# Optimization experiments

Measured on AMD Instinct MI355X. Metric: run time of the kernel, lower is better.

The kernel has to match this reference:

```python
import jax, jax.numpy as jnp
import numpy as np

B, S, D = 2, 2048, 2048
NH, NKV, HD = 16, 4, 128
ROPE_BASE = 10000.0
NEG = -1e9


def _rope_tables(seq_len, dim):
    inv_freq = 1.0 / ROPE_BASE ** (jnp.arange(0, dim, 2, dtype=jnp.float32) / dim)
    t = jnp.arange(seq_len, dtype=jnp.float32)
    freqs = jnp.outer(t, inv_freq)                      # [S, dim/2]
    return jnp.cos(freqs), jnp.sin(freqs)


def _apply_rope(x, cos, sin):
    # x: [B, S, H, HD]; interleaved-pair rotation matching the original module
    x1 = x[..., ::2]
    x2 = x[..., 1::2]
    c = cos[None, :, None, :]
    s = sin[None, :, None, :]
    out1 = x1 * c - x2 * s
    out2 = x1 * s + x2 * c
    return jnp.stack([out1, out2], axis=-1).reshape(x.shape)


def setup_inputs() -> dict:
    key = jax.random.key(0)
    ks = jax.random.split(key, 5)
    x = jax.random.normal(ks[0], (B, S, D), dtype=jnp.float32)
    # causal additive mask [1, 1, S, S]
    causal = jnp.tril(jnp.ones((S, S), dtype=jnp.bool_))
    mask = jnp.where(causal, 0.0, NEG).astype(jnp.float32)[None, None]
    Wq = jax.random.normal(ks[1], (D, NH * HD), dtype=jnp.float32) * (D ** -0.5)
    Wk = jax.random.normal(ks[2], (D, NKV * HD), dtype=jnp.float32) * (D ** -0.5)
    Wv = jax.random.normal(ks[3], (D, NKV * HD), dtype=jnp.float32) * (D ** -0.5)
    Wo = jax.random.normal(ks[4], (NH * HD, D), dtype=jnp.float32) * ((NH * HD) ** -0.5)
    return {"x": x, "mask": mask, "Wq": Wq, "Wk": Wk, "Wv": Wv, "Wo": Wo}


def reference(x, mask, Wq, Wk, Wv, Wo):
    b, s, _ = x.shape
    q = (x @ Wq).reshape(b, s, NH, HD)
    k = (x @ Wk).reshape(b, s, NKV, HD)
    v = (x @ Wv).reshape(b, s, NKV, HD)

    cos, sin = _rope_tables(s, HD)
    q = _apply_rope(q, cos, sin)
    k = _apply_rope(k, cos, sin)

    rep = NH // NKV
    k = jnp.repeat(k, rep, axis=2)                       # [b, s, NH, HD]
    v = jnp.repeat(v, rep, axis=2)

    q = q.transpose(0, 2, 1, 3)                          # [b, NH, s, HD]
    k = k.transpose(0, 2, 1, 3)
    v = v.transpose(0, 2, 1, 3)

    scores = jnp.einsum('bhqd,bhkd->bhqk', q, k) / jnp.sqrt(jnp.float32(HD))
    scores = scores + mask
    attn = jax.nn.softmax(scores, axis=-1)
    out = jnp.einsum('bhqk,bhkd->bhqd', attn, v)
    out = out.transpose(0, 2, 1, 3).reshape(b, s, NH * HD)
    return out @ Wo
```

## Files before the change

kernel.cpp:

```cpp
#include <hip/hip_runtime.h>
#include <stdint.h>

#define B_    2
#define S_    2048
#define D_    2048
#define NH_   16
#define NKV_  4
#define HD_   128
#define M_    (B_*S_)
#define NQKV_ 3072

typedef __bf16 bf16x8 __attribute__((ext_vector_type(8)));
typedef float  f32x4  __attribute__((ext_vector_type(4)));

__device__ __forceinline__ unsigned short f2bf(float f) {
    unsigned int u = __float_as_uint(f);
    u += 0x7fffu + ((u >> 16) & 1u);
    return (unsigned short)(u >> 16);
}

__device__ __forceinline__ unsigned short cvt_bf(float f) {
    __bf16 b = (__bf16)f;
    return *(unsigned short*)&b;
}

__device__ __forceinline__ void async_cp16(const unsigned short* g, unsigned short* l) {
    __builtin_amdgcn_global_load_lds((const __attribute__((address_space(1))) void*)g,
                                     (__attribute__((address_space(3))) void*)l, 16, 0, 0);
}

__global__ void cast_x(const float* __restrict__ x, unsigned short* __restrict__ xb) {
    int idx = blockIdx.x * 256 + threadIdx.x;
    float4 v = ((const float4*)x)[idx];
    unsigned int lo = (unsigned int)f2bf(v.x) | ((unsigned int)f2bf(v.y) << 16);
    unsigned int hi = (unsigned int)f2bf(v.z) | ((unsigned int)f2bf(v.w) << 16);
    ((uint2*)xb)[idx] = make_uint2(lo, hi);
}

__global__ void transpose_cast(const float* __restrict__ src,
                               unsigned short* __restrict__ dst, int ncols) {
    __shared__ float tile[32][33];
    int tx = threadIdx.x, ty = threadIdx.y;
    int n0 = blockIdx.x * 32, k0 = blockIdx.y * 32;
#pragma unroll
    for (int i = 0; i < 4; i++) {
        int k = k0 + ty + i * 8;
        tile[ty + i * 8][tx] = src[(long)k * ncols + n0 + tx];
    }
    __syncthreads();
#pragma unroll
    for (int i = 0; i < 4; i++) {
        int n = n0 + ty + i * 8;
        dst[(long)n * 2048 + k0 + tx] = f2bf(tile[tx][ty + i * 8]);
    }
}

__global__ void rope_tables(float2* __restrict__ ctab) {
    int gid = blockIdx.x * 256 + threadIdx.x;
    int s = gid >> 6, i = gid & 63;
    float inv = exp2f(-(float)i * 0.20762050593046014f);
    float ang = (float)s * inv;
    float sn, cs; sincosf(ang, &sn, &cs);
    ctab[gid] = make_float2(cs, sn);
}


__device__ __forceinline__ bf16x8 lds_frag(const unsigned short* hb, int r, int ks, int quad) {
    int p = (r * 128 + ks * 64 + quad * 16) ^ ((r & 4) << 3);
    return *(const bf16x8*)((const char*)hb + p);
}

__device__ __forceinline__ void stage_half(const unsigned short* g, int Kel,
                                           unsigned short* lhalf, int wid, int lane) {
#pragma unroll
    for (int i = 0; i < 2; i++) {
        int chunk = wid * 2 + i;
        int o = chunk * 1024 + lane * 16;
        int row = o >> 7;
        int cb = (o & 127) ^ ((row & 4) << 3);
        async_cp16((const unsigned short*)((const char*)g + (size_t)row * Kel * 2 + cb),
                   lhalf + chunk * 512);
    }
}

template<int MB, int NB>
__device__ __forceinline__ void cluster(f32x4 (*acc)[4], bf16x8 (*a)[2], bf16x8 (*b)[2]) {
    __builtin_amdgcn_sched_barrier(0);
    __builtin_amdgcn_s_barrier();
    asm volatile("s_waitcnt lgkmcnt(0)" ::: "memory");
    __builtin_amdgcn_sched_barrier(0);
    __builtin_amdgcn_s_setprio(1);
#pragma unroll
    for (int ks = 0; ks < 2; ks++)
#pragma unroll
        for (int mi = 0; mi < 4; mi++)
#pragma unroll
            for (int ni = 0; ni < 2; ni++)
                acc[MB + mi][NB + ni] = __builtin_amdgcn_mfma_f32_16x16x32_bf16(
                    a[mi][ks], b[ni][ks], acc[MB + mi][NB + ni], 0, 0, 0);
    __builtin_amdgcn_s_setprio(0);
    __builtin_amdgcn_sched_barrier(0);
    __builtin_amdgcn_s_barrier();
    __builtin_amdgcn_sched_barrier(0);
}

__device__ __forceinline__ void gemm256_core(const unsigned short* __restrict__ A,
                                             const unsigned short* __restrict__ Bt,
                                             const int K, const int m0, const int n0,
                                             char* sm, f32x4 (*acc)[4]) {
    const int tid  = threadIdx.x;
    const int lane = tid & 63, wid = tid >> 6;
    const int quad = lane >> 4, l16 = lane & 15;
    const int wm = wid >> 2, wn = wid & 3;

    unsigned short* sA00 = (unsigned short*)(sm);
    unsigned short* sA01 = (unsigned short*)(sm + 16384);
    unsigned short* sA10 = (unsigned short*)(sm + 32768);
    unsigned short* sA11 = (unsigned short*)(sm + 49152);
    unsigned short* sB00 = (unsigned short*)(sm + 65536);
    unsigned short* sB01 = (unsigned short*)(sm + 81920);
    unsigned short* sB10 = (unsigned short*)(sm + 98304);
    unsigned short* sB11 = (unsigned short*)(sm + 114688);

    const unsigned short* A0 = A  + (size_t)m0 * K;
    const unsigned short* A1 = A  + (size_t)(m0 + 128) * K;
    const unsigned short* B0 = Bt + (size_t)n0 * K;
    const unsigned short* B1 = Bt + (size_t)(n0 + 128) * K;

    stage_half(A0,      K, sA00, wid, lane);
    stage_half(B1,      K, sB01, wid, lane);
    stage_half(A1,      K, sA01, wid, lane);
    stage_half(B0,      K, sB00, wid, lane);
    __builtin_amdgcn_sched_barrier(0);
    stage_half(A0 + 64, K, sA10, wid, lane);
    stage_half(B1 + 64, K, sB11, wid, lane);
    stage_half(A1 + 64, K, sA11, wid, lane);
    asm volatile("s_waitcnt vmcnt(6)" ::: "memory");
    __builtin_amdgcn_sched_barrier(0);
    __builtin_amdgcn_s_barrier();
    __builtin_amdgcn_sched_barrier(0);

    const int NIT = K >> 7;
    for (int j = 0; j < NIT; ++j) {
        const bool st = (j < NIT - 1);
        const int kof1 = (2 * j + 1) * 64;
        const int kof2 = (2 * j + 2) * 64;
        const int kof3 = (2 * j + 3) * 64;
        bf16x8 af[4][2], bA[2][2], bB[2][2];

#pragma unroll
        for (int mi = 0; mi < 4; mi++)
#pragma unroll
            for (int ks = 0; ks < 2; ks++)
                af[mi][ks] = lds_frag(sA00, wm * 64 + mi * 16 + l16, ks, quad);
#pragma unroll
        for (int ni = 0; ni < 2; ni++)
#pragma unroll
            for (int ks = 0; ks < 2; ks++)
                bA[ni][ks] = lds_frag(sB00, wn * 32 + ni * 16 + l16, ks, quad);
        stage_half(B0 + kof1, K, sB10, wid, lane);
        cluster<0, 0>(acc, af, bA);

#pragma unroll
        for (int ni = 0; ni < 2; ni++)
#pragma unroll
            for (int ks = 0; ks < 2; ks++)
                bB[ni][ks] = lds_frag(sB01, wn * 32 + ni * 16 + l16, ks, quad);
        if (st) stage_half(A0 + kof2, K, sA00, wid, lane);
        cluster<0, 2>(acc, af, bB);

#pragma unroll
        for (int mi = 0; mi < 4; mi++)
#pragma unroll
            for (int ks = 0; ks < 2; ks++)
                af[mi][ks] = lds_frag(sA01, wm * 64 + mi * 16 + l16, ks, quad);
        if (st) stage_half(B1 + kof2, K, sB01, wid, lane);
        cluster<4, 2>(acc, af, bB);

#pragma unroll
        for (int ni = 0; ni < 2; ni++)
#pragma unroll
            for (int ks = 0; ks < 2; ks++)
                bA[ni][ks] = lds_frag(sB00, wn * 32 + ni * 16 + l16, ks, quad);
        if (st) {
            stage_half(A1 + kof2, K, sA01, wid, lane);
            asm volatile("s_waitcnt vmcnt(6)" ::: "memory");
        } else {
            asm volatile("s_waitcnt vmcnt(0)" ::: "memory");
        }
        cluster<4, 0>(acc, af, bA);

#pragma unroll
        for (int mi = 0; mi < 4; mi++)
#pragma unroll
            for (int ks = 0; ks < 2; ks++)
                af[mi][ks] = lds_frag(sA10, wm * 64 + mi * 16 + l16, ks, quad);
#pragma unroll
        for (int ni = 0; ni < 2; ni++)
#pragma unroll
            for (int ks = 0; ks < 2; ks++)
                bA[ni][ks] = lds_frag(sB10, wn * 32 + ni * 16 + l16, ks, quad);
        if (st) stage_half(B0 + kof2, K, sB00, wid, lane);
        cluster<0, 0>(acc, af, bA);

#pragma unroll
        for (int ni = 0; ni < 2; ni++)
#pragma unroll
            for (int ks = 0; ks < 2; ks++)
                bB[ni][ks] = lds_frag(sB11, wn * 32 + ni * 16 + l16, ks, quad);
        if (st) stage_half(A0 + kof3, K, sA10, wid, lane);
        cluster<0, 2>(acc, af, bB);

#pragma unroll
        for (int mi = 0; mi < 4; mi++)
#pragma unroll
            for (int ks = 0; ks < 2; ks++)
                af[mi][ks] = lds_frag(sA11, wm * 64 + mi * 16 + l16, ks, quad);
        if (st) stage_half(B1 + kof3, K, sB11, wid, lane);
        cluster<4, 2>(acc, af, bB);

#pragma unroll
        for (int ni = 0; ni < 2; ni++)
#pragma unroll
            for (int ks = 0; ks < 2; ks++)
                bA[ni][ks] = lds_frag(sB10, wn * 32 + ni * 16 + l16, ks, quad);
        if (st) {
            stage_half(A1 + kof3, K, sA11, wid, lane);
            asm volatile("s_waitcnt vmcnt(6)" ::: "memory");
        }
        cluster<4, 0>(acc, af, bA);
    }
}

__global__ __launch_bounds__(512, 2) void gemm_qkv256(const unsigned short* __restrict__ A,
                                                      const unsigned short* __restrict__ Bt,
                                                      const float2* __restrict__ ctab,
                                                      unsigned short* __restrict__ Qr,
                                                      unsigned short* __restrict__ Kr,
                                                      unsigned short* __restrict__ Vrow) {
    extern __shared__ char sm[];
    const int m0 = blockIdx.y * 256, n0 = blockIdx.x * 256;
    f32x4 acc[8][4] = {};
    gemm256_core(A, Bt, D_, m0, n0, sm, acc);

    const int tid  = threadIdx.x;
    const int lane = tid & 63, wid = tid >> 6;
    const int quad = lane >> 4, l16 = lane & 15;
    const int wm = wid >> 2, wn = wid & 3;

    if (n0 < 2048) {
#pragma unroll
        for (int mt = 0; mt < 8; mt++) {
            int rowb = m0 + ((mt & 4) << 5) + wm * 64 + (mt & 3) * 16 + quad * 4;
#pragma unroll
            for (int nt = 0; nt < 4; nt++) {
                int col = n0 + ((nt & 2) << 6) + wn * 32 + (nt & 1) * 16 + l16;
                int h = col >> 7, d = col & 127;
#pragma unroll
                for (int r = 0; r < 4; r++) {
                    int row = rowb + r;
                    int s = row & 2047, b = row >> 11;
                    float2 cs = ctab[s * 64 + (d >> 1)];
                    float own = acc[mt][nt][r];
                    float other = __shfl_xor(own, 1);
                    float val = (d & 1) ? (other * cs.y + own * cs.x)
                                        : (own * cs.x - other * cs.y);
                    Qr[((size_t)(b * 16 + h) * 2048 + s) * 128 + d] = f2bf(val);
                }
            }
        }
    } else if (n0 < 2560) {
#pragma unroll
        for (int mt = 0; mt < 8; mt++) {
            int rowb = m0 + ((mt & 4) << 5) + wm * 64 + (mt & 3) * 16 + quad * 4;
#pragma unroll
            for (int nt = 0; nt < 4; nt++) {
                int col = n0 + ((nt & 2) << 6) + wn * 32 + (nt & 1) * 16 + l16;
                int kvh = (col - 2048) >> 7, d = col & 127;
#pragma unroll
                for (int r = 0; r < 4; r++) {
                    int row = rowb + r;
                    int s = row & 2047, b = row >> 11;
                    float2 cs = ctab[s * 64 + (d >> 1)];
                    float own = acc[mt][nt][r];
                    float other = __shfl_xor(own, 1);
                    float val = (d & 1) ? (other * cs.y + own * cs.x)
                                        : (own * cs.x - other * cs.y);
                    Kr[((size_t)(b * 4 + kvh) * 2048 + s) * 128 + d] = f2bf(val);
                }
            }
        }
    } else {
#pragma unroll
        for (int mt = 0; mt < 8; mt++) {
            int rowb = m0 + ((mt & 4) << 5) + wm * 64 + (mt & 3) * 16 + quad * 4;
#pragma unroll
            for (int nt = 0; nt < 4; nt++) {
                int col = n0 + ((nt & 2) << 6) + wn * 32 + (nt & 1) * 16 + l16;
#pragma unroll
                for (int r = 0; r < 4; r++)
                    Vrow[(size_t)(rowb + r) * 512 + (col - 2560)] = f2bf(acc[mt][nt][r]);
            }
        }
    }
}

__global__ __launch_bounds__(512, 2) void gemm_bt128x256(const unsigned short* __restrict__ A,
                                                         const unsigned short* __restrict__ Bt,
                                                         float* __restrict__ C) {
    extern __shared__ char sm[];
    const int K = NH_ * HD_;
    const int tid  = threadIdx.x;
    const int lane = tid & 63, wid = tid >> 6;
    const int quad = lane >> 4, l16 = lane & 15;
    const int wm = wid >> 2, wn = wid & 3;
    const int m0 = blockIdx.y * 128, n0 = blockIdx.x * 256;

    unsigned short* sA0  = (unsigned short*)(sm);
    unsigned short* sA1  = (unsigned short*)(sm + 16384);
    unsigned short* sB00 = (unsigned short*)(sm + 32768);
    unsigned short* sB01 = (unsigned short*)(sm + 49152);
    unsigned short* sB10 = (unsigned short*)(sm + 65536);
    unsigned short* sB11 = (unsigned short*)(sm + 81920);

    const unsigned short* A0 = A  + (size_t)m0 * K;
    const unsigned short* B0 = Bt + (size_t)n0 * K;
    const unsigned short* B1 = Bt + (size_t)(n0 + 128) * K;

    f32x4 acc[4][4] = {};

    stage_half(A0,      K, sA0,  wid, lane);
    stage_half(B0,      K, sB00, wid, lane);
    stage_half(B1,      K, sB01, wid, lane);
    __builtin_amdgcn_sched_barrier(0);
    stage_half(A0 + 64, K, sA1,  wid, lane);
    stage_half(B0 + 64, K, sB10, wid, lane);
    asm volatile("s_waitcnt vmcnt(6)" ::: "memory");
    __builtin_amdgcn_sched_barrier(0);
    __builtin_amdgcn_s_barrier();
    __builtin_amdgcn_sched_barrier(0);

    const int NIT = K >> 7;
    for (int j = 0; j < NIT; ++j) {
        const bool st = (j < NIT - 1);
        const int t1 = (2 * j + 1) * 64;
        const int t2 = (2 * j + 2) * 64;
        const int t3 = (2 * j + 3) * 64;
        bf16x8 af[4][2], bb[2][2];

#pragma unroll
        for (int mi = 0; mi < 4; mi++)
#pragma unroll
            for (int ks = 0; ks < 2; ks++)
                af[mi][ks] = lds_frag(sA0, wm * 64 + mi * 16 + l16, ks, quad);
#pragma unroll
        for (int ni = 0; ni < 2; ni++)
#pragma unroll
            for (int ks = 0; ks < 2; ks++)
                bb[ni][ks] = lds_frag(sB00, wn * 32 + ni * 16 + l16, ks, quad);
        stage_half(B1 + t1, K, sB11, wid, lane);
        asm volatile("s_waitcnt vmcnt(6)" ::: "memory");
        cluster<0, 0>(acc, af, bb);

#pragma unroll
        for (int ni = 0; ni < 2; ni++)
#pragma unroll
            for (int ks = 0; ks < 2; ks++)
                bb[ni][ks] = lds_frag(sB01, wn * 32 + ni * 16 + l16, ks, quad);
        if (st) {
            stage_half(A0 + t2, K, sA0,  wid, lane);
            stage_half(B0 + t2, K, sB00, wid, lane);
            asm volatile("s_waitcnt vmcnt(6)" ::: "memory");
        } else {
            asm volatile("s_waitcnt vmcnt(2)" ::: "memory");
        }
        cluster<0, 2>(acc, af, bb);

#pragma unroll
        for (int mi = 0; mi < 4; mi++)
#pragma unroll
            for (int ks = 0; ks < 2; ks++)
                af[mi][ks] = lds_frag(sA1, wm * 64 + mi * 16 + l16, ks, quad);
#pragma unroll
        for (int ni = 0; ni < 2; ni++)
#pragma unroll
            for (int ks = 0; ks < 2; ks++)
                bb[ni][ks] = lds_frag(sB10, wn * 32 + ni * 16 + l16, ks, quad);
        if (st) {
            stage_half(B1 + t2, K, sB01, wid, lane);
            asm volatile("s_waitcnt vmcnt(6)" ::: "memory");
        } else {
            asm volatile("s_waitcnt vmcnt(0)" ::: "memory");
        }
        cluster<0, 0>(acc, af, bb);

#pragma unroll
        for (int ni = 0; ni < 2; ni++)
#pragma unroll
            for (int ks = 0; ks < 2; ks++)
                bb[ni][ks] = lds_frag(sB11, wn * 32 + ni * 16 + l16, ks, quad);
        if (st) {
            stage_half(A0 + t3, K, sA1,  wid, lane);
            stage_half(B0 + t3, K, sB10, wid, lane);
            asm volatile("s_waitcnt vmcnt(6)" ::: "memory");
        }
        cluster<0, 2>(acc, af, bb);
    }

#pragma unroll
    for (int mi = 0; mi < 4; mi++) {
        int rowb = m0 + wm * 64 + mi * 16 + quad * 4;
#pragma unroll
        for (int nb = 0; nb < 2; nb++)
#pragma unroll
            for (int ni = 0; ni < 2; ni++) {
                int col = n0 + nb * 128 + wn * 32 + ni * 16 + l16;
#pragma unroll
                for (int r = 0; r < 4; r++)
                    C[(size_t)(rowb + r) * 2048 + col] = acc[mi][nb * 2 + ni][r];
            }
    }
}

__global__ void v_trans_bf(const unsigned short* __restrict__ Vrow,
                           unsigned short* __restrict__ Vt) {
    __shared__ unsigned short tile[32][34];
    int tx = threadIdx.x, ty = threadIdx.y;
    int s0 = blockIdx.x * 32, d0 = blockIdx.y * 32;
    int bz = blockIdx.z;
    int b = bz >> 2, kvh = bz & 3;
#pragma unroll
    for (int i = 0; i < 4; i++) {
        int s = s0 + ty + i * 8;
        tile[ty + i * 8][tx] = Vrow[(long)(b * 2048 + s) * 512 + kvh * 128 + d0 + tx];
    }
    __syncthreads();
#pragma unroll
    for (int i = 0; i < 4; i++) {
        int d = d0 + ty + i * 8;
        Vt[((long)bz * 128 + d) * 2048 + s0 + tx] = tile[tx][ty + i * 8];
    }
}

__global__ __launch_bounds__(256) void attn_fwd(const unsigned short* __restrict__ Qr,
                                                const unsigned short* __restrict__ Kr,
                                                const unsigned short* __restrict__ Vt,
                                                unsigned short* __restrict__ O) {
    __shared__ char KsB[64 * 256];
    __shared__ char VsB[128 * 128];
    __shared__ unsigned short Ps[4][16][72];
    const int tid  = threadIdx.x;
    const int lane = tid & 63, wid = tid >> 6;
    const int quad = lane >> 4, l16 = lane & 15;
    const int pid = blockIdx.x, h = blockIdx.y, b = blockIdx.z;
    const int kvh = h >> 2;
    const unsigned short* qp = Qr + (long)(b * NH_ + h) * S_ * HD_;
    const char* kpB = (const char*)(Kr + (long)(b * NKV_ + kvh) * S_ * HD_);
    const char* vpB = (const char*)(Vt + (long)(b * NKV_ + kvh) * HD_ * S_);
    const float sc2 = 0.08838834764831845f * 1.4426950408889634f;

    const int wKb = (tid * 16) ^ ((((tid >> 4) & 7)) << 4);
    const int wVb = (tid * 16) ^ ((((tid >> 3) & 7)) << 4);
    const int gKb = tid * 16;
    const int gVb = (tid >> 3) * (S_ * 2) + (tid & 7) * 16;
    int kro[4], vro[2];
#pragma unroll
    for (int ks = 0; ks < 4; ks++)
        kro[ks] = l16 * 256 + ((ks * 64 + quad * 16) ^ ((l16 & 7) << 4));
#pragma unroll
    for (int ks2 = 0; ks2 < 2; ks2++)
        vro[ks2] = l16 * 128 + ((ks2 * 64 + quad * 16) ^ ((l16 & 7) << 4));

    bf16x8 ones;
#pragma unroll
    for (int i = 0; i < 8; i++) ones[i] = (__bf16)1.0f;

    for (int phase = 0; phase < 2; phase++) {
        const int qt = phase ? pid : 31 - pid;
        const int qw = qt * 64 + wid * 16;

        bf16x8 aq[4];
#pragma unroll
        for (int ks = 0; ks < 4; ks++)
            aq[ks] = *(const bf16x8*)&qp[(long)(qw + l16) * HD_ + ks * 32 + quad * 8];

        f32x4 o[8] = {};
        float mi[4], li[4];
#pragma unroll
        for (int r = 0; r < 4; r++) { mi[r] = -3.0e38f; li[r] = 0.f; }

        for (int kt = 0; kt <= qt; kt++) {
            const int kv0 = kt * 64;
            const char* kg = kpB + (size_t)kv0 * 256 + gKb;
            const char* vg = vpB + (size_t)kv0 * 2 + gVb;
            __syncthreads();
#pragma unroll
            for (int i = 0; i < 4; i++)
                *(uint4*)(KsB + wKb + i * 4096) = *(const uint4*)(kg + i * 4096);
#pragma unroll
            for (int i = 0; i < 4; i++)
                *(uint4*)(VsB + wVb + i * 4096) = *(const uint4*)(vg + (size_t)i * 32 * (S_ * 2));
            __syncthreads();

            f32x4 s[4] = {};
#pragma unroll
            for (int ks = 0; ks < 4; ks++)
#pragma unroll
                for (int nt = 0; nt < 4; nt++) {
                    bf16x8 kb = *(const bf16x8*)&KsB[kro[ks] + nt * 4096];
                    s[nt] = __builtin_amdgcn_mfma_f32_16x16x32_bf16(aq[ks], kb, s[nt], 0, 0, 0);
                }

            float mt4[4];
#pragma unroll
            for (int r = 0; r < 4; r++) mt4[r] = -3.0e38f;
            if (kv0 + 63 > qw) {
#pragma unroll
                for (int nt = 0; nt < 4; nt++) {
                    int kvp = kv0 + nt * 16 + l16;
#pragma unroll
                    for (int r = 0; r < 4; r++) {
                        float sv = s[nt][r] * sc2;
                        sv = (kvp <= qw + quad * 4 + r) ? sv : -1.0e30f;
                        s[nt][r] = sv;
                        mt4[r] = fmaxf(mt4[r], sv);
                    }
                }
            } else {
#pragma unroll
                for (int nt = 0; nt < 4; nt++)
#pragma unroll
                    for (int r = 0; r < 4; r++) {
                        float sv = s[nt][r] * sc2;
                        s[nt][r] = sv;
                        mt4[r] = fmaxf(mt4[r], sv);
                    }
            }
#pragma unroll
            for (int off = 1; off < 16; off <<= 1)
#pragma unroll
                for (int r = 0; r < 4; r++)
                    mt4[r] = fmaxf(mt4[r], __shfl_xor(mt4[r], off));

            bool grew = false;
#pragma unroll
            for (int r = 0; r < 4; r++) grew |= (mt4[r] > mi[r]);
            float al[4];
#pragma unroll
            for (int r = 0; r < 4; r++) {
                float mn = fmaxf(mi[r], mt4[r]);
                al[r] = exp2f(mi[r] - mn);
                mi[r] = mn;
            }
            if (__any(grew)) {
#pragma unroll
                for (int t = 0; t < 8; t++)
#pragma unroll
                    for (int r = 0; r < 4; r++) o[t][r] *= al[r];
            }
#pragma unroll
            for (int nt = 0; nt < 4; nt++)
#pragma unroll
                for (int r = 0; r < 4; r++)
                    s[nt][r] = exp2f(s[nt][r] - mi[r]);

#pragma unroll
            for (int nt = 0; nt < 4; nt++)
#pragma unroll
                for (int r = 0; r < 4; r++)
                    Ps[wid][quad * 4 + r][nt * 16 + l16] = cvt_bf(s[nt][r]);

            f32x4 sumf = {};
#pragma unroll
            for (int ks2 = 0; ks2 < 2; ks2++) {
                bf16x8 pa = *(const bf16x8*)&Ps[wid][l16][ks2 * 32 + quad * 8];
                sumf = __builtin_amdgcn_mfma_f32_16x16x32_bf16(pa, ones, sumf, 0, 0, 0);
#pragma unroll
                for (int vt = 0; vt < 8; vt++) {
                    bf16x8 vb = *(const bf16x8*)&VsB[vro[ks2] + vt * 2048];
                    o[vt] = __builtin_amdgcn_mfma_f32_16x16x32_bf16(pa, vb, o[vt], 0, 0, 0);
                }
            }
#pragma unroll
            for (int r = 0; r < 4; r++) li[r] = li[r] * al[r] + sumf[r];
        }

#pragma unroll
        for (int r = 0; r < 4; r++) {
            float inv_l = 1.0f / li[r];
            int qpos = qw + quad * 4 + r;
#pragma unroll
            for (int vt = 0; vt < 8; vt++) {
                float val = o[vt][r] * inv_l;
                O[(long)(b * S_ + qpos) * 2048 + h * 128 + vt * 16 + l16] = cvt_bf(val);
            }
        }
    }
}

extern "C" void kernel_launch(void* const* d_in, const int* in_sizes, int n_in,
                              void* d_out, int out_size, void* d_ws, size_t ws_size,
                              hipStream_t stream) {
    const float* x  = (const float*)d_in[0];
    const float* Wq = (const float*)d_in[2];
    const float* Wk = (const float*)d_in[3];
    const float* Wv = (const float*)d_in[4];
    const float* Wo = (const float*)d_in[5];

    char* ws = (char*)d_ws;
    unsigned short* xb    = (unsigned short*)(ws);
    unsigned short* Wqkvt = (unsigned short*)(ws + 16777216);
    unsigned short* Wot   = (unsigned short*)(ws + 29360128);
    float2*         ctab  = (float2*)        (ws + 37748736);
    unsigned short* Qr    = (unsigned short*)(ws + 38797312);
    unsigned short* Kr    = (unsigned short*)(ws + 55574528);
    unsigned short* Vrow  = (unsigned short*)(ws + 59768832);
    unsigned short* Vt    = (unsigned short*)(ws + 63963136);
    unsigned short* attn  = (unsigned short*)(ws + 68157440);

    static int attr_set = 0;
    if (!attr_set) {
        hipFuncSetAttribute(reinterpret_cast<const void*>(gemm_qkv256),
                            hipFuncAttributeMaxDynamicSharedMemorySize, 131072);
        hipFuncSetAttribute(reinterpret_cast<const void*>(gemm_bt128x256),
                            hipFuncAttributeMaxDynamicSharedMemorySize, 98304);
        attr_set = 1;
    }

    cast_x<<<8192, 256, 0, stream>>>(x, xb);
    dim3 tb(32, 8);
    transpose_cast<<<dim3(64, 64), tb, 0, stream>>>(Wq, Wqkvt, 2048);
    transpose_cast<<<dim3(16, 64), tb, 0, stream>>>(Wk, Wqkvt + 2048 * 2048, 512);
    transpose_cast<<<dim3(16, 64), tb, 0, stream>>>(Wv, Wqkvt + 2560 * 2048, 512);
    transpose_cast<<<dim3(64, 64), tb, 0, stream>>>(Wo, Wot, 2048);
    rope_tables<<<512, 256, 0, stream>>>(ctab);

    gemm_qkv256<<<dim3(12, 16), 512, 131072, stream>>>(xb, Wqkvt, ctab, Qr, Kr, Vrow);

    v_trans_bf<<<dim3(64, 4, 8), tb, 0, stream>>>(Vrow, Vt);

    attn_fwd<<<dim3(16, NH_, B_), 256, 0, stream>>>(Qr, Kr, Vt, attn);

    gemm_bt128x256<<<dim3(8, 32), 512, 98304, stream>>>(attn, Wot, (float*)d_out);
}
```

Baseline: 346.3 us.

## Merge prep kernels into one launch and fuse V transpose into QKV GEMM epilogue

The input cast, the four weight transpose-casts and the RoPE table build now run as one block-indexed prep kernel instead of six launches. The V-projection epilogue of the QKV GEMM writes its tile into swizzled shared memory and stores it transposed, as 16-byte vectors, straight into the Vt layout. This removes the separate V transpose kernel and the Vrow round trip through global memory. It adds a block-wide sync in the GEMM epilogue and reuses the GEMM's shared memory as the transpose buffer.

```diff
diff --git a/kernel.cpp b/kernel.cpp
--- a/kernel.cpp
+++ b/kernel.cpp
@@ -29,39 +29,47 @@
                                      (__attribute__((address_space(3))) void*)l, 16, 0, 0);
 }
 
-__global__ void cast_x(const float* __restrict__ x, unsigned short* __restrict__ xb) {
-    int idx = blockIdx.x * 256 + threadIdx.x;
-    float4 v = ((const float4*)x)[idx];
-    unsigned int lo = (unsigned int)f2bf(v.x) | ((unsigned int)f2bf(v.y) << 16);
-    unsigned int hi = (unsigned int)f2bf(v.z) | ((unsigned int)f2bf(v.w) << 16);
-    ((uint2*)xb)[idx] = make_uint2(lo, hi);
-}
-
-__global__ void transpose_cast(const float* __restrict__ src,
-                               unsigned short* __restrict__ dst, int ncols) {
+__global__ void prep(const float* __restrict__ x, unsigned short* __restrict__ xb,
+                     const float* __restrict__ Wq, const float* __restrict__ Wk,
+                     const float* __restrict__ Wv, const float* __restrict__ Wo,
+                     unsigned short* __restrict__ Wqkvt, unsigned short* __restrict__ Wot,
+                     float2* __restrict__ ctab) {
     __shared__ float tile[32][33];
-    int tx = threadIdx.x, ty = threadIdx.y;
-    int n0 = blockIdx.x * 32, k0 = blockIdx.y * 32;
-#pragma unroll
-    for (int i = 0; i < 4; i++) {
-        int k = k0 + ty + i * 8;
-        tile[ty + i * 8][tx] = src[(long)k * ncols + n0 + tx];
-    }
-    __syncthreads();
-#pragma unroll
-    for (int i = 0; i < 4; i++) {
-        int n = n0 + ty + i * 8;
-        dst[(long)n * 2048 + k0 + tx] = f2bf(tile[tx][ty + i * 8]);
-    }
-}
-
-__global__ void rope_tables(float2* __restrict__ ctab) {
-    int gid = blockIdx.x * 256 + threadIdx.x;
-    int s = gid >> 6, i = gid & 63;
-    float inv = exp2f(-(float)i * 0.20762050593046014f);
-    float ang = (float)s * inv;
-    float sn, cs; sincosf(ang, &sn, &cs);
-    ctab[gid] = make_float2(cs, sn);
+    const int blk = blockIdx.x, tid = threadIdx.x;
+
+    if (blk < 8192) {
+        int idx = blk * 256 + tid;
+        float4 v = ((const float4*)x)[idx];
+        unsigned int lo = (unsigned int)f2bf(v.x) | ((unsigned int)f2bf(v.y) << 16);
+        unsigned int hi = (unsigned int)f2bf(v.z) | ((unsigned int)f2bf(v.w) << 16);
+        ((uint2*)xb)[idx] = make_uint2(lo, hi);
+    } else if (blk < 18432) {
+        const float* src; unsigned short* dst; int ncols, nx, bxy;
+        if (blk < 12288)      { src = Wq; dst = Wqkvt;             ncols = 2048; nx = 64; bxy = blk - 8192; }
+        else if (blk < 13312) { src = Wk; dst = Wqkvt + 2048*2048; ncols = 512;  nx = 16; bxy = blk - 12288; }
+        else if (blk < 14336) { src = Wv; dst = Wqkvt + 2560*2048; ncols = 512;  nx = 16; bxy = blk - 13312; }
+        else                  { src = Wo; dst = Wot;               ncols = 2048; nx = 64; bxy = blk - 14336; }
+        int n0 = (bxy & (nx - 1)) * 32, k0 = (bxy / nx) * 32;
+        int tx = tid & 31, ty = tid >> 5;
+#pragma unroll
+        for (int i = 0; i < 4; i++) {
+            int k = k0 + ty + i * 8;
+            tile[ty + i * 8][tx] = src[(long)k * ncols + n0 + tx];
+        }
+        __syncthreads();
+#pragma unroll
+        for (int i = 0; i < 4; i++) {
+            int n = n0 + ty + i * 8;
+            dst[(long)n * 2048 + k0 + tx] = f2bf(tile[tx][ty + i * 8]);
+        }
+    } else {
+        int gid = (blk - 18432) * 256 + tid;
+        int s = gid >> 6, i = gid & 63;
+        float inv = exp2f(-(float)i * 0.20762050593046014f);
+        float ang = (float)s * inv;
+        float sn, cs; sincosf(ang, &sn, &cs);
+        ctab[gid] = make_float2(cs, sn);
+    }
 }
 
 
@@ -237,7 +245,7 @@
                                                       const float2* __restrict__ ctab,
                                                       unsigned short* __restrict__ Qr,
                                                       unsigned short* __restrict__ Kr,
-                                                      unsigned short* __restrict__ Vrow) {
+                                                      unsigned short* __restrict__ Vt) {
     extern __shared__ char sm[];
     const int m0 = blockIdx.y * 256, n0 = blockIdx.x * 256;
     f32x4 acc[8][4] = {};
@@ -291,16 +299,28 @@
             }
         }
     } else {
+        unsigned short* tr = (unsigned short*)sm;
 #pragma unroll
         for (int mt = 0; mt < 8; mt++) {
-            int rowb = m0 + ((mt & 4) << 5) + wm * 64 + (mt & 3) * 16 + quad * 4;
+            int slb = ((mt & 4) << 5) + wm * 64 + (mt & 3) * 16 + quad * 4;
 #pragma unroll
             for (int nt = 0; nt < 4; nt++) {
-                int col = n0 + ((nt & 2) << 6) + wn * 32 + (nt & 1) * 16 + l16;
+                int cl = ((nt & 2) << 6) + wn * 32 + (nt & 1) * 16 + l16;
 #pragma unroll
                 for (int r = 0; r < 4; r++)
-                    Vrow[(size_t)(rowb + r) * 512 + (col - 2560)] = f2bf(acc[mt][nt][r]);
-            }
+                    tr[cl * 256 + ((slb + r) ^ ((cl & 7) << 3))] = f2bf(acc[mt][nt][r]);
+            }
+        }
+        __syncthreads();
+        const int bb = m0 >> 11, sbase = m0 & 2047;
+#pragma unroll
+        for (int pass = 0; pass < 16; pass++) {
+            int idx = pass * 512 + tid;
+            int cl = idx >> 5, sch = idx & 31;
+            uint4 v = *(const uint4*)&tr[cl * 256 + ((sch * 8) ^ ((cl & 7) << 3))];
+            int col = n0 + cl;
+            int kvh = (col - 2560) >> 7, d = col & 127;
+            *(uint4*)&Vt[((size_t)(bb * 4 + kvh) * 128 + d) * 2048 + sbase + sch * 8] = v;
         }
     }
 }
@@ -419,26 +439,6 @@
                 for (int r = 0; r < 4; r++)
                     C[(size_t)(rowb + r) * 2048 + col] = acc[mi][nb * 2 + ni][r];
             }
-    }
-}
-
-__global__ void v_trans_bf(const unsigned short* __restrict__ Vrow,
-                           unsigned short* __restrict__ Vt) {
-    __shared__ unsigned short tile[32][34];
-    int tx = threadIdx.x, ty = threadIdx.y;
-    int s0 = blockIdx.x * 32, d0 = blockIdx.y * 32;
-    int bz = blockIdx.z;
-    int b = bz >> 2, kvh = bz & 3;
-#pragma unroll
-    for (int i = 0; i < 4; i++) {
-        int s = s0 + ty + i * 8;
-        tile[ty + i * 8][tx] = Vrow[(long)(b * 2048 + s) * 512 + kvh * 128 + d0 + tx];
-    }
-    __syncthreads();
-#pragma unroll
-    for (int i = 0; i < 4; i++) {
-        int d = d0 + ty + i * 8;
-        Vt[((long)bz * 128 + d) * 2048 + s0 + tx] = tile[tx][ty + i * 8];
     }
 }
 
@@ -614,7 +614,6 @@
     float2*         ctab  = (float2*)        (ws + 37748736);
     unsigned short* Qr    = (unsigned short*)(ws + 38797312);
     unsigned short* Kr    = (unsigned short*)(ws + 55574528);
-    unsigned short* Vrow  = (unsigned short*)(ws + 59768832);
     unsigned short* Vt    = (unsigned short*)(ws + 63963136);
     unsigned short* attn  = (unsigned short*)(ws + 68157440);
 
@@ -627,17 +626,9 @@
         attr_set = 1;
     }
 
-    cast_x<<<8192, 256, 0, stream>>>(x, xb);
-    dim3 tb(32, 8);
-    transpose_cast<<<dim3(64, 64), tb, 0, stream>>>(Wq, Wqkvt, 2048);
-    transpose_cast<<<dim3(16, 64), tb, 0, stream>>>(Wk, Wqkvt + 2048 * 2048, 512);
-    transpose_cast<<<dim3(16, 64), tb, 0, stream>>>(Wv, Wqkvt + 2560 * 2048, 512);
-    transpose_cast<<<dim3(64, 64), tb, 0, stream>>>(Wo, Wot, 2048);
-    rope_tables<<<512, 256, 0, stream>>>(ctab);
-
-    gemm_qkv256<<<dim3(12, 16), 512, 131072, stream>>>(xb, Wqkvt, ctab, Qr, Kr, Vrow);
-
-    v_trans_bf<<<dim3(64, 4, 8), tb, 0, stream>>>(Vrow, Vt);
+    prep<<<18944, 256, 0, stream>>>(x, xb, Wq, Wk, Wv, Wo, Wqkvt, Wot, ctab);
+
+    gemm_qkv256<<<dim3(12, 16), 512, 131072, stream>>>(xb, Wqkvt, ctab, Qr, Kr, Vt);
 
     attn_fwd<<<dim3(16, NH_, B_), 256, 0, stream>>>(Qr, Kr, Vt, attn);
 
```

After: 332.8 us. -3.9%, faster.
